# Performance work log

Measured on AMD Instinct MI355X. Metric: run time of the kernel, lower is better.

The kernel has to match this reference:

```python
import jax, jax.numpy as jnp
import numpy as np

TAU = 2.0      # LIF membrane time constant
V_TH = 1.0     # firing threshold (spikingjelly default)
NUM_HEADS = 8

@jax.custom_vjp
def heaviside(x, alpha):
    return (x >= 0.0).astype(x.dtype)

def _hv_fwd(x, alpha):
    return heaviside(x, alpha), (x, alpha)

def _hv_bwd(res, g):
    x, alpha = res
    s = jax.nn.sigmoid(alpha * x)  # sigmoid surrogate gradient
    return (g * alpha * s * (1.0 - s), jnp.zeros_like(alpha))

heaviside.defvjp(_hv_fwd, _hv_bwd)

def lif(x_seq, alpha):
    """Multi-step LIF over leading time dim. Hard reset to 0, detach_reset."""
    def step(v, x):
        h = v + (x - v) / TAU
        s = heaviside(h - V_TH, alpha)
        v_new = h * (1.0 - jax.lax.stop_gradient(s))
        return v_new, s
    _, spikes = jax.lax.scan(step, jnp.zeros_like(x_seq[0]), x_seq)
    return spikes

def bn1d(x, gamma, beta, mean, var, eps=1e-5):
    # x: [TB, C, N]; inference-mode BatchNorm1d over channel dim
    inv = gamma / jnp.sqrt(var + eps)
    return x * inv[None, :, None] + (beta - mean * inv)[None, :, None]

def setup_inputs():
    T, B, C, H, W = 4, 32, 384, 16, 16
    key = jax.random.key(0)
    ks = jax.random.split(key, 6)
    w = lambda k: jax.random.normal(k, (C, C), jnp.float32) * (1.0 / np.sqrt(C))
    ones = jnp.ones((C,), jnp.float32)
    zeros = jnp.zeros((C,), jnp.float32)
    return dict(
        x=jax.random.normal(ks[0], (T, B, C, H, W), jnp.float32),
        alpha=jnp.float32(2.0),
        q_w=w(ks[1]), q_gamma=ones, q_beta=zeros, q_mean=zeros, q_var=ones,
        k_w=w(ks[2]), k_gamma=ones, k_beta=zeros, k_mean=zeros, k_var=ones,
        v_w=w(ks[3]), v_gamma=ones, v_beta=zeros, v_mean=zeros, v_var=ones,
        proj_w=w(ks[4]), proj_b=jax.random.normal(ks[5], (C,), jnp.float32) * 0.01,
        p_gamma=ones, p_beta=zeros, p_mean=zeros, p_var=ones,
    )

def reference(x, alpha, q_w, q_gamma, q_beta, q_mean, q_var,
              k_w, k_gamma, k_beta, k_mean, k_var,
              v_w, v_gamma, v_beta, v_mean, v_var,
              proj_w, proj_b, p_gamma, p_beta, p_mean, p_var):
    T, B, C, H, W = x.shape
    N = H * W
    d = C // NUM_HEADS

    s = lif(x, alpha).reshape(T, B, C, N)         # proj_lif + flatten(3)
    xf = s.reshape(T * B, C, N)                   # flatten(0,1)

    def branch(w_, g_, b_, m_, v_):
        y = jnp.einsum('oc,bcn->bon', w_, xf)     # conv1x1
        y = bn1d(y, g_, b_, m_, v_).reshape(T, B, C, N)
        y = lif(y, alpha)
        # [T,B,C,N] -> [T,B,N,C] -> [T,B,N,h,d] -> [T,B,h,N,d]
        return y.transpose(0, 1, 3, 2).reshape(T, B, N, NUM_HEADS, d).transpose(0, 1, 3, 2, 4)

    q = branch(q_w, q_gamma, q_beta, q_mean, q_var)
    k = branch(k_w, k_gamma, k_beta, k_mean, k_var)
    v = branch(v_w, v_gamma, v_beta, v_mean, v_var)

    attn = jnp.einsum('tbhnd,tbhmd->tbhnm', q, k)          # q @ k^T (no softmax)
    out = jnp.einsum('tbhnm,tbhmd->tbhnd', attn, v) * 0.125
    # transpose(3,4) then reshape -> [T,B,C,N] (head-major channel layout)
    out = out.transpose(0, 1, 2, 4, 3).reshape(T, B, C, N)
    out = lif(out, alpha)                                  # attn_lif

    of = out.reshape(T * B, C, N)
    y = jnp.einsum('oc,bcn->bon', proj_w, of) + proj_b[None, :, None]
    y = bn1d(y, p_gamma, p_beta, p_mean, p_var)
    return y.reshape(T, B, C, H, W)
```

## Files before the change

kernel.cpp:

```cpp
#include <hip/hip_runtime.h>
#include <hip/hip_bf16.h>

#define T_  4
#define B_  32
#define C_  384
#define N_  256
#define NH_ 8
#define D_  48

typedef __attribute__((ext_vector_type(8))) short bf16x8;
typedef __attribute__((ext_vector_type(4))) float f32x4;

__device__ __forceinline__ float bf2f(unsigned short s) {
    return __uint_as_float(((unsigned int)s) << 16);
}
__device__ __forceinline__ unsigned short f2bf(float f) {
    __hip_bfloat16 h = __float2bfloat16(f);
    return __builtin_bit_cast(unsigned short, h);
}

__global__ __launch_bounds__(256) void k_wsplit(const float* __restrict__ w0,
                                                const float* __restrict__ w1,
                                                const float* __restrict__ w2,
                                                const float* __restrict__ w3,
                                                unsigned short* __restrict__ hi,
                                                unsigned short* __restrict__ lo) {
    const float* w = (blockIdx.y==0) ? w0 : (blockIdx.y==1) ? w1 : (blockIdx.y==2) ? w2 : w3;
    int g = blockIdx.x*256 + threadIdx.x;
    int otile = g / 768;
    int rem = g - otile*768;
    int lane = rem & 63;
    int o  = otile*16 + (lane & 15);
    int k0 = (rem >> 6)*32 + (lane >> 4)*8;
    const float* src = w + (size_t)o*C_ + k0;
    unsigned short h8[8], l8[8];
    #pragma unroll
    for (int j=0;j<8;++j) {
        float f = src[j];
        h8[j] = f2bf(f);
        l8[j] = f2bf(f - bf2f(h8[j]));
    }
    size_t dst = (size_t)blockIdx.y*147456 + (size_t)g*8;
    *(uint4*)(hi + dst) = *(uint4*)h8;
    *(uint4*)(lo + dst) = *(uint4*)l8;
}

__global__ __launch_bounds__(256) void k_lif1(const float* __restrict__ x,
                                              unsigned char* __restrict__ s0b) {
    __shared__ unsigned short Tt[64*72];
    const int tid = threadIdx.x;
    const int b  = blockIdx.x;
    const int c0 = blockIdx.y * 64;
    const int n0 = blockIdx.z * 64;
    const int ci = tid >> 2;
    const int nj = (tid & 3) * 16;
    float v[16];
    #pragma unroll
    for (int i=0;i<16;++i) v[i]=0.f;
    for (int t = 0; t < T_; ++t) {
        const float* xp = x + (((size_t)t*B_ + b)*C_ + c0 + ci)*N_ + n0 + nj;
        #pragma unroll
        for (int q=0;q<4;++q) {
            float4 f = *(const float4*)(xp + q*4);
            float e[4] = {f.x,f.y,f.z,f.w};
            #pragma unroll
            for (int j=0;j<4;++j) {
                int ii = q*4+j;
                float h = v[ii] + (e[j] - v[ii])*0.5f;
                bool sp = (h - 1.0f) >= 0.f;
                v[ii] = sp ? 0.f : h;
                Tt[(nj + ii)*72 + ci] = sp ? 0x3F80u : 0u;
            }
        }
        __syncthreads();
        #pragma unroll
        for (int half=0; half<2; ++half) {
            int e = tid + half*256;
            int nl = e >> 3, cbyte = e & 7;
            unsigned short tmp[8];
            *(uint4*)tmp = *(const uint4*)&Tt[nl*72 + cbyte*8];
            unsigned byte = 0;
            #pragma unroll
            for (int j=0;j<8;++j) byte |= (tmp[j] ? 1u : 0u) << j;
            int n = n0 + nl, c = c0 + cbyte*8;
            int ks = c >> 5, kc = (c >> 3) & 3;
            size_t dst = ((((size_t)(t*B_ + b)*16 + (n>>4))*12 + ks)*64) + kc*16 + (n & 15);
            s0b[dst] = (unsigned char)byte;
        }
        __syncthreads();
    }
}

struct Br2 {
    const unsigned short* whi[3];
    const unsigned short* wlo[3];
    const float *g[3], *be[3], *me[3], *va[3];
    unsigned char* outb[3];
};

__global__ __launch_bounds__(256, 2) void k_branch(const unsigned char* __restrict__ s0b, Br2 a) {
    __shared__ float Ep[32*260];
    __shared__ float BNi[128], BNo[128];
    __shared__ unsigned short LUT[2048];
    const int tid = threadIdx.x;
    const int z  = blockIdx.z;
    const int o0 = blockIdx.y * 128;
    const int bx = blockIdx.x;
    const int b  = bx >> 2;
    const int n0 = (bx & 3) * 64;
    const int nt0 = bx & 3;
    const int w    = tid >> 6;
    const int lane = tid & 63;
    const int quad = lane >> 4;
    const int lc   = lane & 15;
    const unsigned short* __restrict__ Wgh = a.whi[z];
    const unsigned short* __restrict__ Wgl = a.wlo[z];

    #pragma unroll
    for (int j=0;j<8;++j) LUT[tid*8 + j] = ((tid >> j) & 1) ? 0x3F80u : 0u;
    if (tid < 128) {
        int o = o0 + tid;
        float inv = a.g[z][o] / sqrtf(a.va[z][o] + 1e-5f);
        BNi[tid] = inv;
        BNo[tid] = a.be[z][o] - a.me[z][o]*inv;
    }
    __syncthreads();

    const int base_ot = (o0 >> 4) + (w >> 1)*4;
    const unsigned short* pAh[4];
    const unsigned short* pAl[4];
    const unsigned char* pBY[8];
    #pragma unroll
    for (int mt=0;mt<4;++mt) {
        size_t off = (size_t)(base_ot + mt)*6144 + lane*8;
        pAh[mt] = Wgh + off;
        pAl[mt] = Wgl + off;
    }
    #pragma unroll
    for (int nt=0;nt<8;++nt) {
        int cb = (w&1)*128 + nt*16;
        int t = cb >> 6;
        int ntile = (n0 >> 4) + ((cb & 63) >> 4);
        pBY[nt] = s0b + ((size_t)(t*B_ + b)*16 + ntile)*768 + lane;
    }

    f32x4 acc[4][8];
    #pragma unroll
    for (int mt=0;mt<4;++mt)
        #pragma unroll
        for (int nt=0;nt<8;++nt) { acc[mt][nt][0]=0.f; acc[mt][nt][1]=0.f; acc[mt][nt][2]=0.f; acc[mt][nt][3]=0.f; }

    #pragma unroll
    for (int ks = 0; ks < 12; ++ks) {
        bf16x8 ah[4], al[4], bb[8];
        unsigned char byt[8];
        #pragma unroll
        for (int nt=0;nt<8;++nt) { byt[nt] = *(pBY[nt]); pBY[nt] += 64; }
        #pragma unroll
        for (int mt=0;mt<4;++mt) {
            ah[mt] = *(const bf16x8*)(pAh[mt]); pAh[mt] += 512;
            al[mt] = *(const bf16x8*)(pAl[mt]); pAl[mt] += 512;
        }
        #pragma unroll
        for (int nt=0;nt<8;++nt) bb[nt] = *(const bf16x8*)&LUT[(int)byt[nt]*8];
        #pragma unroll
        for (int mt=0;mt<4;++mt)
            #pragma unroll
            for (int nt=0;nt<8;++nt) {
                acc[mt][nt] = __builtin_amdgcn_mfma_f32_16x16x32_bf16(ah[mt], bb[nt], acc[mt][nt], 0,0,0);
                acc[mt][nt] = __builtin_amdgcn_mfma_f32_16x16x32_bf16(al[mt], bb[nt], acc[mt][nt], 0,0,0);
            }
    }

    unsigned char* outb = a.outb[z];
    for (int r = 0; r < 4; ++r) {
        __syncthreads();
        int erow = (w>>1)*16 + quad*4;
        #pragma unroll
        for (int nt=0;nt<8;++nt) {
            int col = (w&1)*128 + nt*16 + lc;
            Ep[(erow+0)*260 + col] = acc[r][nt][0];
            Ep[(erow+1)*260 + col] = acc[r][nt][1];
            Ep[(erow+2)*260 + col] = acc[r][nt][2];
            Ep[(erow+3)*260 + col] = acc[r][nt][3];
        }
        __syncthreads();
        {
            int orow = tid >> 3;
            int ns8 = (tid & 7) * 8;
            int oloc = ((orow & 16) ? 64 : 0) + r*16 + (orow & 15);
            int o = o0 + oloc;
            float inv = BNi[oloc], off = BNo[oloc];
            float v[8];
            #pragma unroll
            for (int j=0;j<8;++j) v[j]=0.f;
            #pragma unroll
            for (int t=0;t<4;++t) {
                float4 f0 = *(const float4*)&Ep[orow*260 + t*64 + ns8];
                float4 f1 = *(const float4*)&Ep[orow*260 + t*64 + ns8 + 4];
                float e[8] = {f0.x,f0.y,f0.z,f0.w,f1.x,f1.y,f1.z,f1.w};
                unsigned byte = 0;
                #pragma unroll
                for (int j=0;j<8;++j) {
                    float y = e[j]*inv + off;
                    float h = v[j] + (y - v[j])*0.5f;
                    bool sp = (h - 1.0f) >= 0.f;
                    v[j] = sp ? 0.f : h;
                    byte |= (sp ? 1u : 0u) << j;
                }
                outb[(((size_t)(t*B_ + b)*4 + nt0)*C_ + o)*8 + (tid & 7)] = (unsigned char)byte;
            }
        }
    }
}

__global__ __launch_bounds__(256) void k_attn(const unsigned char* __restrict__ qb,
                                              const unsigned char* __restrict__ kb,
                                              const unsigned char* __restrict__ vb,
                                              unsigned char* __restrict__ s2b) {
    __shared__ unsigned short Qt[256*72];
    __shared__ unsigned short KtVb[48*72];
    __shared__ unsigned long long KB[192], VB[192], QB[192];
    const int tid = threadIdx.x;
    const int w = tid >> 6, lane = tid & 63, quad = lane >> 4, lc = lane & 15;
    const int bh = blockIdx.x;
    const int b  = bh >> 3, hh = bh & 7;

    *(uint4*)&Qt[tid*72 + 48] = make_uint4(0,0,0,0);
    *(uint4*)&Qt[tid*72 + 56] = make_uint4(0,0,0,0);
    if (tid < 48) {
        *(uint4*)&KtVb[tid*72 + 48] = make_uint4(0,0,0,0);
        *(uint4*)&KtVb[tid*72 + 56] = make_uint4(0,0,0,0);
    }

    float vst[4][3][4];
    #pragma unroll
    for (int j=0;j<4;++j)
        #pragma unroll
        for (int nt=0;nt<3;++nt)
            #pragma unroll
            for (int r=0;r<4;++r) vst[j][nt][r]=0.f;

    for (int t = 0; t < T_; ++t) {
        __syncthreads();
        if (tid < 192) {
            int dd = tid >> 2, j = tid & 3;
            size_t src = (((size_t)(t*B_ + b)*4 + j)*C_ + hh*D_ + dd)*8;
            KB[tid] = *(const unsigned long long*)(kb + src);
            VB[tid] = *(const unsigned long long*)(vb + src);
            QB[tid] = *(const unsigned long long*)(qb + src);
        }
        __syncthreads();
        {
            int q64 = tid >> 6, sh = tid & 63;
            #pragma unroll
            for (int dd=0; dd<48; ++dd)
                Qt[tid*72 + dd] = ((QB[dd*4 + q64] >> sh) & 1ULL) ? 0x3F80u : 0u;
        }
        #pragma unroll
        for (int i=0;i<9;++i) {
            int p = tid + i*256;
            if (p < 2304) {
                int dd1 = p / 48, dd2 = p - dd1*48;
                const unsigned long long* kr = &KB[dd1*4];
                const unsigned long long* vr = &VB[dd2*4];
                int c = __popcll(kr[0]&vr[0]) + __popcll(kr[1]&vr[1])
                      + __popcll(kr[2]&vr[2]) + __popcll(kr[3]&vr[3]);
                KtVb[dd2*72 + dd1] = f2bf((float)c);
            }
        }
        __syncthreads();
        f32x4 acc2[4][3];
        #pragma unroll
        for (int j=0;j<4;++j)
            #pragma unroll
            for (int nt=0;nt<3;++nt) { acc2[j][nt][0]=0.f; acc2[j][nt][1]=0.f; acc2[j][nt][2]=0.f; acc2[j][nt][3]=0.f; }
        #pragma unroll
        for (int k2=0; k2<2; ++k2) {
            bf16x8 bfr[3];
            #pragma unroll
            for (int nt=0;nt<3;++nt)
                bfr[nt] = *(const bf16x8*)&KtVb[(nt*16 + lc)*72 + k2*32 + quad*8];
            #pragma unroll
            for (int j=0;j<4;++j) {
                bf16x8 af = *(const bf16x8*)&Qt[((w*4 + j)*16 + lc)*72 + k2*32 + quad*8];
                #pragma unroll
                for (int nt=0;nt<3;++nt)
                    acc2[j][nt] = __builtin_amdgcn_mfma_f32_16x16x32_bf16(af, bfr[nt], acc2[j][nt], 0,0,0);
            }
        }
        #pragma unroll
        for (int j=0;j<4;++j) {
            int nr = (w*4 + j)*16 + quad*4;
            #pragma unroll
            for (int nt=0;nt<3;++nt)
                #pragma unroll
                for (int r=0;r<4;++r) {
                    float y = acc2[j][nt][r]*0.125f;
                    float vv = vst[j][nt][r];
                    float h = vv + (y - vv)*0.5f;
                    bool s = (h - 1.0f) >= 0.f;
                    vst[j][nt][r] = s ? 0.f : h;
                    Qt[(nr + r)*72 + nt*16 + lc] = s ? 0x3F80u : 0u;
                }
        }
        __syncthreads();
        {
            #pragma unroll
            for (int c8=0; c8<6; ++c8) {
                unsigned short tmp[8];
                *(uint4*)tmp = *(const uint4*)&Qt[tid*72 + c8*8];
                unsigned byte = 0;
                #pragma unroll
                for (int j=0;j<8;++j) byte |= (tmp[j] ? 1u : 0u) << j;
                int ci = hh*6 + c8;
                int ks = ci >> 2, kc = ci & 3;
                size_t dst = ((((size_t)(t*B_ + b)*16 + (tid>>4))*12 + ks)*64) + kc*16 + (tid & 15);
                s2b[dst] = (unsigned char)byte;
            }
        }
    }
}

__global__ __launch_bounds__(256, 2) void k_proj(const unsigned char* __restrict__ s2b,
        const unsigned short* __restrict__ Wgh, const unsigned short* __restrict__ Wgl,
        const float* __restrict__ pb,
        const float* __restrict__ g, const float* __restrict__ be,
        const float* __restrict__ me, const float* __restrict__ va,
        float* __restrict__ out) {
    __shared__ float Ep[32*260];
    __shared__ float BNi[128], BNo[128];
    __shared__ unsigned short LUT[2048];
    const int tid = threadIdx.x;
    const int o0 = blockIdx.y * 128;
    const int bx = blockIdx.x;
    const int b  = bx >> 2;
    const int n0 = (bx & 3) * 64;
    const int w    = tid >> 6;
    const int lane = tid & 63;
    const int quad = lane >> 4;
    const int lc   = lane & 15;

    #pragma unroll
    for (int j=0;j<8;++j) LUT[tid*8 + j] = ((tid >> j) & 1) ? 0x3F80u : 0u;
    if (tid < 128) {
        int o = o0 + tid;
        float inv = g[o] / sqrtf(va[o] + 1e-5f);
        BNi[tid] = inv;
        BNo[tid] = be[o] - me[o]*inv + pb[o]*inv;
    }
    __syncthreads();

    const int base_ot = (o0 >> 4) + (w >> 1)*4;
    const unsigned short* pAh[4];
    const unsigned short* pAl[4];
    const unsigned char* pBY[8];
    #pragma unroll
    for (int mt=0;mt<4;++mt) {
        size_t off = (size_t)(base_ot + mt)*6144 + lane*8;
        pAh[mt] = Wgh + off;
        pAl[mt] = Wgl + off;
    }
    #pragma unroll
    for (int nt=0;nt<8;++nt) {
        int cb = (w&1)*128 + nt*16;
        int t = cb >> 6;
        int ntile = (n0 >> 4) + ((cb & 63) >> 4);
        pBY[nt] = s2b + ((size_t)(t*B_ + b)*16 + ntile)*768 + lane;
    }

    f32x4 acc[4][8];
    #pragma unroll
    for (int mt=0;mt<4;++mt)
        #pragma unroll
        for (int nt=0;nt<8;++nt) { acc[mt][nt][0]=0.f; acc[mt][nt][1]=0.f; acc[mt][nt][2]=0.f; acc[mt][nt][3]=0.f; }

    #pragma unroll
    for (int ks = 0; ks < 12; ++ks) {
        bf16x8 ah[4], al[4], bb[8];
        unsigned char byt[8];
        #pragma unroll
        for (int nt=0;nt<8;++nt) { byt[nt] = *(pBY[nt]); pBY[nt] += 64; }
        #pragma unroll
        for (int mt=0;mt<4;++mt) {
            ah[mt] = *(const bf16x8*)(pAh[mt]); pAh[mt] += 512;
            al[mt] = *(const bf16x8*)(pAl[mt]); pAl[mt] += 512;
        }
        #pragma unroll
        for (int nt=0;nt<8;++nt) bb[nt] = *(const bf16x8*)&LUT[(int)byt[nt]*8];
        #pragma unroll
        for (int mt=0;mt<4;++mt)
            #pragma unroll
            for (int nt=0;nt<8;++nt) {
                acc[mt][nt] = __builtin_amdgcn_mfma_f32_16x16x32_bf16(ah[mt], bb[nt], acc[mt][nt], 0,0,0);
                acc[mt][nt] = __builtin_amdgcn_mfma_f32_16x16x32_bf16(al[mt], bb[nt], acc[mt][nt], 0,0,0);
            }
    }

    for (int r = 0; r < 4; ++r) {
        __syncthreads();
        int erow = (w>>1)*16 + quad*4;
        #pragma unroll
        for (int nt=0;nt<8;++nt) {
            int col = (w&1)*128 + nt*16 + lc;
            Ep[(erow+0)*260 + col] = acc[r][nt][0];
            Ep[(erow+1)*260 + col] = acc[r][nt][1];
            Ep[(erow+2)*260 + col] = acc[r][nt][2];
            Ep[(erow+3)*260 + col] = acc[r][nt][3];
        }
        __syncthreads();
        #pragma unroll
        for (int q=0;q<8;++q) {
            int e = q*256 + tid;
            int orow = e >> 6;
            int rem = e & 63;
            int t = rem >> 4, nq = rem & 15;
            int oloc = ((orow & 16) ? 64 : 0) + r*16 + (orow & 15);
            int o = o0 + oloc;
            float4 f = *(const float4*)&Ep[orow*260 + t*64 + nq*4];
            float inv = BNi[oloc], off = BNo[oloc];
            float4 rr = make_float4(f.x*inv+off, f.y*inv+off, f.z*inv+off, f.w*inv+off);
            *(float4*)(out + (((size_t)t*B_ + b)*C_ + o)*N_ + n0 + nq*4) = rr;
        }
    }
}

extern "C" void kernel_launch(void* const* d_in, const int* in_sizes, int n_in,
                              void* d_out, int out_size, void* d_ws, size_t ws_size,
                              hipStream_t stream) {
    const float* x  = (const float*)d_in[0];
    char* ws = (char*)d_ws;
    unsigned char* S0B = (unsigned char*)ws;
    unsigned char* QB = (unsigned char*)(ws + 2097152);
    unsigned char* KB = (unsigned char*)(ws + 4194304);
    unsigned char* VB = (unsigned char*)(ws + 6291456);
    unsigned char* S2B = (unsigned char*)(ws + 8388608);
    unsigned short* WHI = (unsigned short*)(ws + 100663296);
    unsigned short* WLO = WHI + 4*147456;

    k_wsplit<<<dim3(72,4), 256, 0, stream>>>(
        (const float*)d_in[2], (const float*)d_in[7], (const float*)d_in[12],
        (const float*)d_in[17], WHI, WLO);

    k_lif1<<<dim3(32,6,4), 256, 0, stream>>>(x, S0B);

    Br2 ba;
    for (int z=0;z<3;++z) { ba.whi[z] = WHI + z*147456; ba.wlo[z] = WLO + z*147456; }
    ba.g[0]=(const float*)d_in[3];  ba.be[0]=(const float*)d_in[4];
    ba.me[0]=(const float*)d_in[5]; ba.va[0]=(const float*)d_in[6];
    ba.g[1]=(const float*)d_in[8];  ba.be[1]=(const float*)d_in[9];
    ba.me[1]=(const float*)d_in[10]; ba.va[1]=(const float*)d_in[11];
    ba.g[2]=(const float*)d_in[13]; ba.be[2]=(const float*)d_in[14];
    ba.me[2]=(const float*)d_in[15]; ba.va[2]=(const float*)d_in[16];
    ba.outb[0]=QB; ba.outb[1]=KB; ba.outb[2]=VB;
    k_branch<<<dim3(128, 3, 3), 256, 0, stream>>>(S0B, ba);

    k_attn<<<B_*NH_, 256, 0, stream>>>(QB, KB, VB, S2B);

    k_proj<<<dim3(128, 3), 256, 0, stream>>>(S2B,
        WHI + 3*147456, WLO + 3*147456,
        (const float*)d_in[18],
        (const float*)d_in[19], (const float*)d_in[20],
        (const float*)d_in[21], (const float*)d_in[22],
        (float*)d_out);
}
```

Baseline: 226.2 us.

## Halve GEMM block N-tile in branch and proj kernels to double grid size

The branch and projection GEMM kernels now cover 128 output columns per block instead of 256, so the grid doubles and accumulator registers drop from 32 to 16 tiles per wave. This gives more blocks to fill the CUs and may raise occupancy. In exchange the weight tiles are reloaded by twice as many blocks. The packed spike layout for Q/K/V changes to 32-wide groups, and the attention kernel's loads are rewritten to assemble 64-bit masks from two 32-bit pieces.

```diff
diff --git a/kernel.cpp b/kernel.cpp
--- a/kernel.cpp
+++ b/kernel.cpp
@@ -99,16 +99,16 @@
 };
 
 __global__ __launch_bounds__(256, 2) void k_branch(const unsigned char* __restrict__ s0b, Br2 a) {
-    __shared__ float Ep[32*260];
+    __shared__ float Ep[32*132];
     __shared__ float BNi[128], BNo[128];
     __shared__ unsigned short LUT[2048];
     const int tid = threadIdx.x;
     const int z  = blockIdx.z;
     const int o0 = blockIdx.y * 128;
     const int bx = blockIdx.x;
-    const int b  = bx >> 2;
-    const int n0 = (bx & 3) * 64;
-    const int nt0 = bx & 3;
+    const int b  = bx >> 3;
+    const int n0 = (bx & 7) * 32;
+    const int g32 = n0 >> 5;
     const int w    = tid >> 6;
     const int lane = tid & 63;
     const int quad = lane >> 4;
@@ -129,7 +129,7 @@
     const int base_ot = (o0 >> 4) + (w >> 1)*4;
     const unsigned short* pAh[4];
     const unsigned short* pAl[4];
-    const unsigned char* pBY[8];
+    const unsigned char* pBY[4];
     #pragma unroll
     for (int mt=0;mt<4;++mt) {
         size_t off = (size_t)(base_ot + mt)*6144 + lane*8;
@@ -137,36 +137,36 @@
         pAl[mt] = Wgl + off;
     }
     #pragma unroll
-    for (int nt=0;nt<8;++nt) {
-        int cb = (w&1)*128 + nt*16;
-        int t = cb >> 6;
-        int ntile = (n0 >> 4) + ((cb & 63) >> 4);
+    for (int nt=0;nt<4;++nt) {
+        int cb = (w&1)*64 + nt*16;
+        int t = cb >> 5;
+        int ntile = (n0 >> 4) + ((cb >> 4) & 1);
         pBY[nt] = s0b + ((size_t)(t*B_ + b)*16 + ntile)*768 + lane;
     }
 
-    f32x4 acc[4][8];
+    f32x4 acc[4][4];
     #pragma unroll
     for (int mt=0;mt<4;++mt)
         #pragma unroll
-        for (int nt=0;nt<8;++nt) { acc[mt][nt][0]=0.f; acc[mt][nt][1]=0.f; acc[mt][nt][2]=0.f; acc[mt][nt][3]=0.f; }
+        for (int nt=0;nt<4;++nt) { acc[mt][nt][0]=0.f; acc[mt][nt][1]=0.f; acc[mt][nt][2]=0.f; acc[mt][nt][3]=0.f; }
 
     #pragma unroll
     for (int ks = 0; ks < 12; ++ks) {
-        bf16x8 ah[4], al[4], bb[8];
-        unsigned char byt[8];
-        #pragma unroll
-        for (int nt=0;nt<8;++nt) { byt[nt] = *(pBY[nt]); pBY[nt] += 64; }
+        bf16x8 ah[4], al[4], bb[4];
+        unsigned char byt[4];
+        #pragma unroll
+        for (int nt=0;nt<4;++nt) { byt[nt] = *(pBY[nt]); pBY[nt] += 64; }
         #pragma unroll
         for (int mt=0;mt<4;++mt) {
             ah[mt] = *(const bf16x8*)(pAh[mt]); pAh[mt] += 512;
             al[mt] = *(const bf16x8*)(pAl[mt]); pAl[mt] += 512;
         }
         #pragma unroll
-        for (int nt=0;nt<8;++nt) bb[nt] = *(const bf16x8*)&LUT[(int)byt[nt]*8];
+        for (int nt=0;nt<4;++nt) bb[nt] = *(const bf16x8*)&LUT[(int)byt[nt]*8];
         #pragma unroll
         for (int mt=0;mt<4;++mt)
             #pragma unroll
-            for (int nt=0;nt<8;++nt) {
+            for (int nt=0;nt<4;++nt) {
                 acc[mt][nt] = __builtin_amdgcn_mfma_f32_16x16x32_bf16(ah[mt], bb[nt], acc[mt][nt], 0,0,0);
                 acc[mt][nt] = __builtin_amdgcn_mfma_f32_16x16x32_bf16(al[mt], bb[nt], acc[mt][nt], 0,0,0);
             }
@@ -177,17 +177,17 @@
         __syncthreads();
         int erow = (w>>1)*16 + quad*4;
         #pragma unroll
-        for (int nt=0;nt<8;++nt) {
-            int col = (w&1)*128 + nt*16 + lc;
-            Ep[(erow+0)*260 + col] = acc[r][nt][0];
-            Ep[(erow+1)*260 + col] = acc[r][nt][1];
-            Ep[(erow+2)*260 + col] = acc[r][nt][2];
-            Ep[(erow+3)*260 + col] = acc[r][nt][3];
-        }
-        __syncthreads();
-        {
-            int orow = tid >> 3;
-            int ns8 = (tid & 7) * 8;
+        for (int nt=0;nt<4;++nt) {
+            int col = (w&1)*64 + nt*16 + lc;
+            Ep[(erow+0)*132 + col] = acc[r][nt][0];
+            Ep[(erow+1)*132 + col] = acc[r][nt][1];
+            Ep[(erow+2)*132 + col] = acc[r][nt][2];
+            Ep[(erow+3)*132 + col] = acc[r][nt][3];
+        }
+        __syncthreads();
+        if (tid < 128) {
+            int orow = tid >> 2;
+            int bidx = tid & 3;
             int oloc = ((orow & 16) ? 64 : 0) + r*16 + (orow & 15);
             int o = o0 + oloc;
             float inv = BNi[oloc], off = BNo[oloc];
@@ -196,8 +196,8 @@
             for (int j=0;j<8;++j) v[j]=0.f;
             #pragma unroll
             for (int t=0;t<4;++t) {
-                float4 f0 = *(const float4*)&Ep[orow*260 + t*64 + ns8];
-                float4 f1 = *(const float4*)&Ep[orow*260 + t*64 + ns8 + 4];
+                float4 f0 = *(const float4*)&Ep[orow*132 + t*32 + bidx*8];
+                float4 f1 = *(const float4*)&Ep[orow*132 + t*32 + bidx*8 + 4];
                 float e[8] = {f0.x,f0.y,f0.z,f0.w,f1.x,f1.y,f1.z,f1.w};
                 unsigned byte = 0;
                 #pragma unroll
@@ -208,7 +208,7 @@
                     v[j] = sp ? 0.f : h;
                     byte |= (sp ? 1u : 0u) << j;
                 }
-                outb[(((size_t)(t*B_ + b)*4 + nt0)*C_ + o)*8 + (tid & 7)] = (unsigned char)byte;
+                outb[(((size_t)(t*B_ + b)*8 + g32)*C_ + o)*4 + bidx] = (unsigned char)byte;
             }
         }
     }
@@ -244,11 +244,15 @@
     for (int t = 0; t < T_; ++t) {
         __syncthreads();
         if (tid < 192) {
-            int dd = tid >> 2, j = tid & 3;
-            size_t src = (((size_t)(t*B_ + b)*4 + j)*C_ + hh*D_ + dd)*8;
-            KB[tid] = *(const unsigned long long*)(kb + src);
-            VB[tid] = *(const unsigned long long*)(vb + src);
-            QB[tid] = *(const unsigned long long*)(qb + src);
+            int dd = tid >> 2, w64 = tid & 3;
+            size_t s0 = (((size_t)(t*B_ + b)*8 + 2*w64)*C_ + hh*D_ + dd)*4;
+            size_t s1 = s0 + (size_t)C_*4;
+            KB[tid] = (unsigned long long)*(const unsigned int*)(kb + s0)
+                    | ((unsigned long long)*(const unsigned int*)(kb + s1) << 32);
+            VB[tid] = (unsigned long long)*(const unsigned int*)(vb + s0)
+                    | ((unsigned long long)*(const unsigned int*)(vb + s1) << 32);
+            QB[tid] = (unsigned long long)*(const unsigned int*)(qb + s0)
+                    | ((unsigned long long)*(const unsigned int*)(qb + s1) << 32);
         }
         __syncthreads();
         {
@@ -328,14 +332,15 @@
         const float* __restrict__ g, const float* __restrict__ be,
         const float* __restrict__ me, const float* __restrict__ va,
         float* __restrict__ out) {
-    __shared__ float Ep[32*260];
+    __shared__ float Ep[32*132];
     __shared__ float BNi[128], BNo[128];
     __shared__ unsigned short LUT[2048];
     const int tid = threadIdx.x;
     const int o0 = blockIdx.y * 128;
     const int bx = blockIdx.x;
-    const int b  = bx >> 2;
-    const int n0 = (bx & 3) * 64;
+    const int t  = bx >> 6;
+    const int b  = (bx >> 1) & 31;
+    const int n0 = (bx & 1) * 128;
     const int w    = tid >> 6;
     const int lane = tid & 63;
     const int quad = lane >> 4;
@@ -354,7 +359,7 @@
     const int base_ot = (o0 >> 4) + (w >> 1)*4;
     const unsigned short* pAh[4];
     const unsigned short* pAl[4];
-    const unsigned char* pBY[8];
+    const unsigned char* pBY[4];
     #pragma unroll
     for (int mt=0;mt<4;++mt) {
         size_t off = (size_t)(base_ot + mt)*6144 + lane*8;
@@ -362,36 +367,35 @@
         pAl[mt] = Wgl + off;
     }
     #pragma unroll
-    for (int nt=0;nt<8;++nt) {
-        int cb = (w&1)*128 + nt*16;
-        int t = cb >> 6;
-        int ntile = (n0 >> 4) + ((cb & 63) >> 4);
+    for (int nt=0;nt<4;++nt) {
+        int cb = (w&1)*64 + nt*16;
+        int ntile = (n0 >> 4) + (cb >> 4);
         pBY[nt] = s2b + ((size_t)(t*B_ + b)*16 + ntile)*768 + lane;
     }
 
-    f32x4 acc[4][8];
+    f32x4 acc[4][4];
     #pragma unroll
     for (int mt=0;mt<4;++mt)
         #pragma unroll
-        for (int nt=0;nt<8;++nt) { acc[mt][nt][0]=0.f; acc[mt][nt][1]=0.f; acc[mt][nt][2]=0.f; acc[mt][nt][3]=0.f; }
+        for (int nt=0;nt<4;++nt) { acc[mt][nt][0]=0.f; acc[mt][nt][1]=0.f; acc[mt][nt][2]=0.f; acc[mt][nt][3]=0.f; }
 
     #pragma unroll
     for (int ks = 0; ks < 12; ++ks) {
-        bf16x8 ah[4], al[4], bb[8];
-        unsigned char byt[8];
-        #pragma unroll
-        for (int nt=0;nt<8;++nt) { byt[nt] = *(pBY[nt]); pBY[nt] += 64; }
+        bf16x8 ah[4], al[4], bb[4];
+        unsigned char byt[4];
+        #pragma unroll
+        for (int nt=0;nt<4;++nt) { byt[nt] = *(pBY[nt]); pBY[nt] += 64; }
         #pragma unroll
         for (int mt=0;mt<4;++mt) {
             ah[mt] = *(const bf16x8*)(pAh[mt]); pAh[mt] += 512;
             al[mt] = *(const bf16x8*)(pAl[mt]); pAl[mt] += 512;
         }
         #pragma unroll
-        for (int nt=0;nt<8;++nt) bb[nt] = *(const bf16x8*)&LUT[(int)byt[nt]*8];
+        for (int nt=0;nt<4;++nt) bb[nt] = *(const bf16x8*)&LUT[(int)byt[nt]*8];
         #pragma unroll
         for (int mt=0;mt<4;++mt)
             #pragma unroll
-            for (int nt=0;nt<8;++nt) {
+            for (int nt=0;nt<4;++nt) {
                 acc[mt][nt] = __builtin_amdgcn_mfma_f32_16x16x32_bf16(ah[mt], bb[nt], acc[mt][nt], 0,0,0);
                 acc[mt][nt] = __builtin_amdgcn_mfma_f32_16x16x32_bf16(al[mt], bb[nt], acc[mt][nt], 0,0,0);
             }
@@ -401,23 +405,22 @@
         __syncthreads();
         int erow = (w>>1)*16 + quad*4;
         #pragma unroll
-        for (int nt=0;nt<8;++nt) {
-            int col = (w&1)*128 + nt*16 + lc;
-            Ep[(erow+0)*260 + col] = acc[r][nt][0];
-            Ep[(erow+1)*260 + col] = acc[r][nt][1];
-            Ep[(erow+2)*260 + col] = acc[r][nt][2];
-            Ep[(erow+3)*260 + col] = acc[r][nt][3];
-        }
-        __syncthreads();
-        #pragma unroll
-        for (int q=0;q<8;++q) {
+        for (int nt=0;nt<4;++nt) {
+            int col = (w&1)*64 + nt*16 + lc;
+            Ep[(erow+0)*132 + col] = acc[r][nt][0];
+            Ep[(erow+1)*132 + col] = acc[r][nt][1];
+            Ep[(erow+2)*132 + col] = acc[r][nt][2];
+            Ep[(erow+3)*132 + col] = acc[r][nt][3];
+        }
+        __syncthreads();
+        #pragma unroll
+        for (int q=0;q<4;++q) {
             int e = q*256 + tid;
-            int orow = e >> 6;
-            int rem = e & 63;
-            int t = rem >> 4, nq = rem & 15;
+            int orow = e >> 5;
+            int nq = e & 31;
             int oloc = ((orow & 16) ? 64 : 0) + r*16 + (orow & 15);
             int o = o0 + oloc;
-            float4 f = *(const float4*)&Ep[orow*260 + t*64 + nq*4];
+            float4 f = *(const float4*)&Ep[orow*132 + nq*4];
             float inv = BNi[oloc], off = BNo[oloc];
             float4 rr = make_float4(f.x*inv+off, f.y*inv+off, f.z*inv+off, f.w*inv+off);
             *(float4*)(out + (((size_t)t*B_ + b)*C_ + o)*N_ + n0 + nq*4) = rr;
@@ -453,11 +456,11 @@
     ba.g[2]=(const float*)d_in[13]; ba.be[2]=(const float*)d_in[14];
     ba.me[2]=(const float*)d_in[15]; ba.va[2]=(const float*)d_in[16];
     ba.outb[0]=QB; ba.outb[1]=KB; ba.outb[2]=VB;
-    k_branch<<<dim3(128, 3, 3), 256, 0, stream>>>(S0B, ba);
+    k_branch<<<dim3(256, 3, 3), 256, 0, stream>>>(S0B, ba);
 
     k_attn<<<B_*NH_, 256, 0, stream>>>(QB, KB, VB, S2B);
 
-    k_proj<<<dim3(128, 3), 256, 0, stream>>>(S2B,
+    k_proj<<<dim3(256, 3), 256, 0, stream>>>(S2B,
         WHI + 3*147456, WLO + 3*147456,
         (const float*)d_in[18],
         (const float*)d_in[19], (const float*)d_in[20],
```

Measured after the change: 217.8 us. 1.04x faster.
